# Performance work log

Measured on AMD Instinct MI355X. Metric: run time of the kernel, lower is better.

## Reference

```python
import jax, jax.numpy as jnp
import numpy as np

B, S, F, L = 128, 512, 128, 1024  # batch, seq_len, n_features, latent_dim


def _gru_step(h, x, W_ih, W_hh, b_ih, b_hh):
    # PyTorch GRUCell math, gate order (r, z, n)
    gi = x @ W_ih.T + b_ih            # [B, 3L]
    gh = h @ W_hh.T + b_hh            # [B, 3L]
    ir, iz, inn = jnp.split(gi, 3, axis=-1)
    hr, hz, hn = jnp.split(gh, 3, axis=-1)
    r = jax.nn.sigmoid(ir + hr)
    z = jax.nn.sigmoid(iz + hz)
    n = jnp.tanh(inn + r * hn)
    return (1.0 - z) * n + z * h


def setup_inputs() -> dict:
    key = jax.random.key(0)
    ks = jax.random.split(key, 12)
    s_e = 1.0 / np.sqrt(L)
    u = lambda k, shape: jax.random.uniform(k, shape, jnp.float32, -s_e, s_e)
    return {
        "x": jax.random.normal(ks[0], (B, S, F), jnp.float32),
        # encoder GRU (single layer)
        "W_ih_e": u(ks[1], (3 * L, F)),
        "W_hh_e": u(ks[2], (3 * L, L)),
        "b_ih_e": u(ks[3], (3 * L,)),
        "b_hh_e": u(ks[4], (3 * L,)),
        # decoder GRUCell
        "W_ih_d": u(ks[5], (3 * L, F)),
        "W_hh_d": u(ks[6], (3 * L, L)),
        "b_ih_d": u(ks[7], (3 * L,)),
        "b_hh_d": u(ks[8], (3 * L,)),
        # decoder Linear(latent_dim -> n_features)
        "W_out": u(ks[9], (F, L)),
        "b_out": u(ks[10], (F,)),
    }


def reference(x, W_ih_e, W_hh_e, b_ih_e, b_hh_e,
              W_ih_d, W_hh_d, b_ih_d, b_hh_d, W_out, b_out):
    seq_len = x.shape[1]

    # ---- encoder: GRU over time, return final hidden state h_n [B, L] ----
    def enc_step(h, x_t):
        h = _gru_step(h, x_t, W_ih_e, W_hh_e, b_ih_e, b_hh_e)
        return h, None

    h0 = jnp.zeros((x.shape[0], W_hh_e.shape[1]), x.dtype)
    h_n, _ = jax.lax.scan(enc_step, h0, jnp.swapaxes(x, 0, 1))  # scan over [S,B,F]

    # ---- decoder: GRUCell + Linear unrolled seq_len steps ----
    x_init = h_n @ W_out.T + b_out  # [B, F]

    def dec_step(carry, _):
        h, x_i = carry
        h = _gru_step(h, x_i, W_ih_d, W_hh_d, b_ih_d, b_hh_d)
        x_i = h @ W_out.T + b_out
        return (h, x_i), x_i

    _, xs = jax.lax.scan(dec_step, (h_n, x_init), None, length=seq_len)  # [S,B,F]
    out = jnp.swapaxes(xs, 0, 1)  # [B,S,F]
    return jnp.flip(out, axis=1)
```

## Files before the change

kernel.cpp:

```cpp
#include <hip/hip_runtime.h>
#include <hip/hip_bf16.h>


#define B_ 128
#define S_ 512
#define F_ 128
#define L_ 1024
#define U_ 8
#define NWG_E 128
#define NWG_D 144

typedef __bf16 bf16x8 __attribute__((ext_vector_type(8)));
typedef float  f32x4  __attribute__((ext_vector_type(4)));
typedef float  f32x16 __attribute__((ext_vector_type(16)));
typedef int    i32x4  __attribute__((ext_vector_type(4)));
typedef unsigned long long u64;

union pk2 { unsigned u; __bf16 h[2]; };
union fu  { float f; unsigned u; };

#define MFMA32(a, b, c) __builtin_amdgcn_mfma_f32_32x32x16_bf16(a, b, c, 0, 0, 0)
#define Z16 f32x16{0.f,0.f,0.f,0.f,0.f,0.f,0.f,0.f,0.f,0.f,0.f,0.f,0.f,0.f,0.f,0.f}

#define LDG16(dst, p) asm volatile("global_load_dwordx4 %0, %1, off sc0 sc1" : "=v"(dst) : "v"(p))
#define VMWAIT16(a) asm volatile("s_waitcnt vmcnt(0)" \
    : "+v"(a[0]),"+v"(a[1]),"+v"(a[2]),"+v"(a[3]),"+v"(a[4]),"+v"(a[5]),"+v"(a[6]),"+v"(a[7]), \
      "+v"(a[8]),"+v"(a[9]),"+v"(a[10]),"+v"(a[11]),"+v"(a[12]),"+v"(a[13]),"+v"(a[14]),"+v"(a[15]) \
    :: "memory")
#define SB0() __builtin_amdgcn_sched_barrier(0)

#define O_H0   0
#define O_H1   (256*1024)
#define O_H32  (512*1024)
#define O_CTR  (1024*1024)
#define O_ZERO_END (1024*1024 + 8192)
#define O_XB   O_ZERO_END
#define O_WEH  (O_XB  + 16777216)
#define O_WEX  (O_WEH + 8388608)
#define O_BE   (O_WEX + 1048576)
#define O_WD   (O_BE  + 16384)
#define O_BD   (O_WD  + 8388608)
#define O_WC   (O_BD  + 16384)
#define O_WOB  (O_WC  + 6291456)


__global__ void k_xcvt(const float* __restrict__ x, __bf16* __restrict__ xb, int n) {
    int i = blockIdx.x * 256 + threadIdx.x;
    int stride = gridDim.x * 256;
    for (; i < n; i += stride) xb[i] = (__bf16)x[i];
}

__global__ void k_woutb(const float* __restrict__ Wout, __bf16* __restrict__ Wob, int n) {
    int i = blockIdx.x * 256 + threadIdx.x;
    if (i < n) Wob[i] = (__bf16)Wout[i];
}

__global__ void k_pack_enc(const float* __restrict__ Wih, const float* __restrict__ Whh,
                           const float* __restrict__ bih, const float* __restrict__ bhh,
                           __bf16* __restrict__ Weh, __bf16* __restrict__ Wex,
                           float* __restrict__ be) {
    int g = blockIdx.x, tid = threadIdx.x;
    for (int i = tid; i < 32 * 1024; i += 256) {
        int c = i >> 10, k = i & 1023;
        int u = g * U_ + (c >> 2), gate = c & 3;
        float v = 0.f;
        if (gate == 0)      v = Whh[(size_t)u * 1024 + k];
        else if (gate == 1) v = Whh[(size_t)(1024 + u) * 1024 + k];
        else if (gate == 3) v = Whh[(size_t)(2048 + u) * 1024 + k];
        Weh[((size_t)g * 32 + c) * 1024 + k] = (__bf16)v;
    }
    for (int i = tid; i < 32 * 128; i += 256) {
        int c = i >> 7, k = i & 127;
        int u = g * U_ + (c >> 2), gate = c & 3;
        float v = 0.f;
        if (gate == 0)      v = Wih[(size_t)u * 128 + k];
        else if (gate == 1) v = Wih[(size_t)(1024 + u) * 128 + k];
        else if (gate == 2) v = Wih[(size_t)(2048 + u) * 128 + k];
        Wex[((size_t)g * 32 + c) * 128 + k] = (__bf16)v;
    }
    if (tid < 32) {
        int c = tid, u = g * U_ + (c >> 2), gate = c & 3;
        float v;
        if (gate == 0)      v = bih[u] + bhh[u];
        else if (gate == 1) v = bih[1024 + u] + bhh[1024 + u];
        else if (gate == 2) v = bih[2048 + u];
        else                v = bhh[2048 + u];
        be[g * 32 + c] = v;
    }
}

__global__ void k_wcomb(const float* __restrict__ Wihd, const float* __restrict__ Wout,
                        __bf16* __restrict__ Wc) {
    __shared__ float a[8][128];
    int r0 = blockIdx.x * 8, tid = threadIdx.x;
    for (int i = tid; i < 8 * 128; i += 256)
        a[i >> 7][i & 127] = Wihd[(size_t)(r0 + (i >> 7)) * 128 + (i & 127)];
    __syncthreads();
    for (int j = tid; j < 1024; j += 256) {
        float acc[8] = {0, 0, 0, 0, 0, 0, 0, 0};
        for (int f = 0; f < 128; ++f) {
            float w = Wout[(size_t)f * 1024 + j];
#pragma unroll
            for (int r = 0; r < 8; ++r) acc[r] += a[r][f] * w;
        }
        for (int r = 0; r < 8; ++r) Wc[(size_t)(r0 + r) * 1024 + j] = (__bf16)acc[r];
    }
}

__global__ void k_pack_dec(const float* __restrict__ Whhd, const __bf16* __restrict__ Wc,
                           const float* __restrict__ Wihd,
                           const float* __restrict__ bihd, const float* __restrict__ bhhd,
                           const float* __restrict__ bout,
                           __bf16* __restrict__ Wd, float* __restrict__ bd) {
    int g = blockIdx.x, tid = threadIdx.x;
    for (int i = tid; i < 32 * 1024; i += 256) {
        int c = i >> 10, k = i & 1023;
        int u = g * U_ + (c >> 2), gate = c & 3;
        float v;
        if (gate == 0)      v = Whhd[(size_t)u * 1024 + k] + (float)Wc[(size_t)u * 1024 + k];
        else if (gate == 1) v = Whhd[(size_t)(1024 + u) * 1024 + k] + (float)Wc[(size_t)(1024 + u) * 1024 + k];
        else if (gate == 2) v = (float)Wc[(size_t)(2048 + u) * 1024 + k];
        else                v = Whhd[(size_t)(2048 + u) * 1024 + k];
        Wd[((size_t)g * 32 + c) * 1024 + k] = (__bf16)v;
    }
    if (tid < 32) {
        int c = tid;
        int u = g * U_ + (c >> 2), gate = c & 3;
        int row = (gate == 0) ? u : (gate == 1) ? (1024 + u) : (2048 + u);
        float v;
        if (gate <= 1) {
            float d = 0.f;
            for (int f = 0; f < 128; ++f) d += Wihd[(size_t)row * 128 + f] * bout[f];
            v = d + bihd[row] + bhhd[row];
        } else if (gate == 2) {
            float d = 0.f;
            for (int f = 0; f < 128; ++f) d += Wihd[(size_t)row * 128 + f] * bout[f];
            v = d + bihd[row];
        } else {
            v = bhhd[row];
        }
        bd[g * 32 + c] = v;
    }
}


__device__ __forceinline__ void bar_arrive(unsigned* base, int g) {
    if (threadIdx.x == 0)
        __hip_atomic_fetch_add(base + (g & 15) * 32, 1u,
                               __ATOMIC_RELAXED, __HIP_MEMORY_SCOPE_AGENT);
}

__device__ __forceinline__ void bar_wait(unsigned* base, unsigned tgt) {
    if (threadIdx.x == 0) {
        for (;;) {
            unsigned sum = 0;
#pragma unroll
            for (int j = 0; j < 16; ++j)
                sum += __hip_atomic_load(base + j * 32, __ATOMIC_RELAXED, __HIP_MEMORY_SCOPE_AGENT);
            if (sum >= tgt) break;
            __builtin_amdgcn_s_sleep(1);
        }
    }
    __syncthreads();
}

__global__ __launch_bounds__(512, 2) void k_enc(
    const __bf16* __restrict__ xb, const __bf16* __restrict__ Weh,
    const __bf16* __restrict__ Wex, const float* __restrict__ be,
    __bf16* __restrict__ h0, __bf16* __restrict__ h1,
    float* __restrict__ h32, unsigned* __restrict__ ctr) {
    __shared__ __align__(16) __bf16 sWh[32][1032];
    __shared__ __align__(16) __bf16 sWx[32][136];
    __shared__ float sB[32];
    __shared__ __align__(16) float sGa[128][36];
    __shared__ __align__(16) float sGb[128][36];
    const int g = blockIdx.x, tid = threadIdx.x;
    const int lane = tid & 63, wave = tid >> 6;

    for (int i = tid; i < 32 * 128; i += 512) {
        int c = i >> 7, k8 = i & 127;
        *(i32x4*)&sWh[c][k8 * 8] = *(const i32x4*)(Weh + ((size_t)g * 32 + c) * 1024 + k8 * 8);
    }
    for (int i = tid; i < 32 * 16; i += 512) {
        int c = i >> 4, k8 = i & 15;
        *(i32x4*)&sWx[c][k8 * 8] = *(const i32x4*)(Wex + ((size_t)g * 32 + c) * 128 + k8 * 8);
    }
    if (tid < 32) sB[tid] = be[g * 32 + tid];
    __syncthreads();

    const int bcol = lane & 31;
    const int koff = (lane >> 5) * 8;
    const int mrow = (wave & 3) * 32 + bcol;
    const int kb = (wave >> 2) * 32;
    const bool up = (wave >= 4);

    bf16x8 xrg[8];
    if (up) {
#pragma unroll
        for (int kt = 0; kt < 8; ++kt) xrg[kt] = *(const bf16x8*)(&sWx[bcol][kt * 16 + koff]);
    }

    const int erow = tid >> 2, pair = tid & 3;
    const int hidx2 = g * 512 + erow * 4 + pair;
    float ha = 0.f, hb = 0.f;

    f32x16 accx = Z16;
    if (up) {
        const __bf16* xr = xb + (size_t)mrow * 65536;
#pragma unroll
        for (int kt = 0; kt < 8; ++kt)
            accx = MFMA32(*(const bf16x8*)(xr + kt * 16 + koff), xrg[kt], accx);
    }

    for (int s = 0; s < 512; ++s) {
        const __bf16* hcur = (s & 1) ? h1 : h0;
        __bf16* hnxt = (s & 1) ? h0 : h1;
        {
            f32x16 aA = up ? accx : Z16;
            f32x16 aB = Z16;
            const __bf16* hr = hcur + ((size_t)(kb * 2 + (koff >> 3)) << 10) + mrow * 8;
            bf16x8 af[16];
#pragma unroll
            for (int i = 0; i < 16; ++i) LDG16(af[i], hr + i * 2048);
            VMWAIT16(af); SB0();
#pragma unroll
            for (int i = 0; i < 16; ++i) {
                const bf16x8 b = *(const bf16x8*)(&sWh[bcol][(kb + i) * 16 + koff]);
                if (i & 1) aB = MFMA32(af[i], b, aB); else aA = MFMA32(af[i], b, aA);
                LDG16(af[i], hr + (16 + i) * 2048);
            }
            VMWAIT16(af); SB0();
#pragma unroll
            for (int i = 0; i < 16; ++i) {
                const bf16x8 b = *(const bf16x8*)(&sWh[bcol][(kb + 16 + i) * 16 + koff]);
                if (i & 1) aB = MFMA32(af[i], b, aB); else aA = MFMA32(af[i], b, aA);
            }
            f32x16 acc = aA + aB;
            int rb = (wave & 3) * 32 + 4 * (lane >> 5);
            float (*sg)[36] = up ? sGb : sGa;
#pragma unroll
            for (int r = 0; r < 16; ++r)
                sg[rb + (r & 3) + 8 * (r >> 2)][bcol] = acc[r];
        }
        __syncthreads();
        {
            f32x4 g0 = *(const f32x4*)&sGa[erow][pair * 8] + *(const f32x4*)&sGb[erow][pair * 8];
            f32x4 g1 = *(const f32x4*)&sGa[erow][pair * 8 + 4] + *(const f32x4*)&sGb[erow][pair * 8 + 4];
            int c0 = pair * 8;
            float r = 1.f / (1.f + __expf(-(g0[0] + sB[c0 + 0])));
            float z = 1.f / (1.f + __expf(-(g0[1] + sB[c0 + 1])));
            float n = tanhf(g0[2] + sB[c0 + 2] + r * (g0[3] + sB[c0 + 3]));
            ha = (1.f - z) * n + z * ha;
            r = 1.f / (1.f + __expf(-(g1[0] + sB[c0 + 4])));
            z = 1.f / (1.f + __expf(-(g1[1] + sB[c0 + 5])));
            n = tanhf(g1[2] + sB[c0 + 6] + r * (g1[3] + sB[c0 + 7]));
            hb = (1.f - z) * n + z * hb;
            pk2 p; p.h[0] = (__bf16)ha; p.h[1] = (__bf16)hb;
            __hip_atomic_store((unsigned*)hnxt + hidx2, p.u, __ATOMIC_RELAXED, __HIP_MEMORY_SCOPE_AGENT);
            if (s == 511) {
                h32[erow * 1024 + g * 8 + pair * 2]     = ha;
                h32[erow * 1024 + g * 8 + pair * 2 + 1] = hb;
            }
        }
        if (s < 511) {
            __syncthreads();
            bar_arrive(ctr, g);
            if (up) {
                f32x16 ax = Z16;
                const __bf16* xr = xb + (size_t)mrow * 65536 + (size_t)(s + 1) * 128;
#pragma unroll
                for (int kt = 0; kt < 8; ++kt)
                    ax = MFMA32(*(const bf16x8*)(xr + kt * 16 + koff), xrg[kt], ax);
                accx = ax;
            }
            bar_wait(ctr, (unsigned)(s + 1) * NWG_E);
        }
    }
}

__global__ __launch_bounds__(512, 2) void k_dec(
    const __bf16* __restrict__ Wd, const float* __restrict__ bd,
    const __bf16* __restrict__ Wob, const float* __restrict__ bout,
    __bf16* __restrict__ h0, __bf16* __restrict__ h1,
    const float* __restrict__ h32, float* __restrict__ out,
    unsigned* __restrict__ ctr) {
    __shared__ __align__(16) __bf16 sW[32][1032];
    __shared__ float sB[32];
    __shared__ __align__(16) float sGa[128][36];
    __shared__ __align__(16) float sGb[128][36];
    const int g = blockIdx.x, tid = threadIdx.x;
    const int lane = tid & 63, wave = tid >> 6;
    const bool gwg = (g < 128);
    const int go = g - 128;

    if (gwg) {
        for (int i = tid; i < 32 * 128; i += 512) {
            int c = i >> 7, k8 = i & 127;
            *(i32x4*)&sW[c][k8 * 8] = *(const i32x4*)(Wd + ((size_t)g * 32 + c) * 1024 + k8 * 8);
        }
        if (tid < 32) sB[tid] = bd[g * 32 + tid];
    } else {
        for (int i = tid; i < 32 * 128; i += 512) {
            int c = i >> 7, k8 = i & 127;
            *(i32x4*)&sW[c][k8 * 8] =
                *(const i32x4*)(Wob + ((size_t)((go >> 2) * 32 + c)) * 1024 + k8 * 8);
        }
        if (tid < 32) sB[tid] = bout[(go >> 2) * 32 + tid];
    }
    __syncthreads();

    const int bcol = lane & 31;
    const int koff = (lane >> 5) * 8;
    const int kb = (wave >> 2) * 32;
    const bool up = (wave >= 4);
    const int arow = gwg ? ((wave & 3) * 32 + bcol)
                         : ((go & 3) * 32 + bcol);

    const int erow = tid >> 2, pair = tid & 3;
    const int hidx2 = g * 512 + erow * 4 + pair;
    float ha = 0.f, hb = 0.f;
    if (gwg) {
        ha = h32[erow * 1024 + g * 8 + pair * 2];
        hb = h32[erow * 1024 + g * 8 + pair * 2 + 1];
    }

    if (gwg) {
        for (int s = 0; s < 512; ++s) {
            const __bf16* hcur = (s & 1) ? h1 : h0;
            __bf16* hnxt = (s & 1) ? h0 : h1;
            {
                f32x16 aA = Z16, aB = Z16;
                const __bf16* hr = hcur + ((size_t)(kb * 2 + (koff >> 3)) << 10) + arow * 8;
                bf16x8 af[16];
#pragma unroll
                for (int i = 0; i < 16; ++i) LDG16(af[i], hr + i * 2048);
                VMWAIT16(af); SB0();
#pragma unroll
                for (int i = 0; i < 16; ++i) {
                    const bf16x8 b = *(const bf16x8*)(&sW[bcol][(kb + i) * 16 + koff]);
                    if (i & 1) aB = MFMA32(af[i], b, aB); else aA = MFMA32(af[i], b, aA);
                    LDG16(af[i], hr + (16 + i) * 2048);
                }
                VMWAIT16(af); SB0();
#pragma unroll
                for (int i = 0; i < 16; ++i) {
                    const bf16x8 b = *(const bf16x8*)(&sW[bcol][(kb + 16 + i) * 16 + koff]);
                    if (i & 1) aB = MFMA32(af[i], b, aB); else aA = MFMA32(af[i], b, aA);
                }
                f32x16 acc = aA + aB;
                int rb = (wave & 3) * 32 + 4 * (lane >> 5);
                float (*sg)[36] = up ? sGb : sGa;
#pragma unroll
                for (int r = 0; r < 16; ++r)
                    sg[rb + (r & 3) + 8 * (r >> 2)][bcol] = acc[r];
            }
            __syncthreads();
            {
                f32x4 g0 = *(const f32x4*)&sGa[erow][pair * 8] + *(const f32x4*)&sGb[erow][pair * 8];
                f32x4 g1 = *(const f32x4*)&sGa[erow][pair * 8 + 4] + *(const f32x4*)&sGb[erow][pair * 8 + 4];
                int c0 = pair * 8;
                float r = 1.f / (1.f + __expf(-(g0[0] + sB[c0 + 0])));
                float z = 1.f / (1.f + __expf(-(g0[1] + sB[c0 + 1])));
                float n = tanhf(g0[2] + sB[c0 + 2] + r * (g0[3] + sB[c0 + 3]));
                ha = (1.f - z) * n + z * ha;
                r = 1.f / (1.f + __expf(-(g1[0] + sB[c0 + 4])));
                z = 1.f / (1.f + __expf(-(g1[1] + sB[c0 + 5])));
                n = tanhf(g1[2] + sB[c0 + 6] + r * (g1[3] + sB[c0 + 7]));
                hb = (1.f - z) * n + z * hb;
                pk2 p; p.h[0] = (__bf16)ha; p.h[1] = (__bf16)hb;
                __hip_atomic_store((unsigned*)hnxt + hidx2, p.u, __ATOMIC_RELAXED, __HIP_MEMORY_SCOPE_AGENT);
            }
            __syncthreads();
            bar_arrive(ctr, g);
            if (s < 511) bar_wait(ctr, (unsigned)(s + 1) * NWG_D);
        }
    } else {
        __shared__ __align__(16) float sGo[4][32][32];
        for (int s = 0; s <= 512; ++s) {
            const __bf16* hcur = (s & 1) ? h1 : h0;
            const bool cmp = (wave < 4) && (s >= 1);
            if (cmp) {
                f32x16 aA = Z16, aB = Z16;
                const __bf16* hr = hcur + ((size_t)(wave * 32 + (koff >> 3)) << 10) + arow * 8;
                bf16x8 af[16];
#pragma unroll
                for (int i = 0; i < 16; ++i) LDG16(af[i], hr + i * 2048);
                VMWAIT16(af); SB0();
#pragma unroll
                for (int i = 0; i < 16; ++i) {
                    const bf16x8 b = *(const bf16x8*)(&sW[bcol][(wave * 16 + i) * 16 + koff]);
                    if (i & 1) aB = MFMA32(af[i], b, aB); else aA = MFMA32(af[i], b, aA);
                }
                f32x16 acc = aA + aB;
                int rb = 4 * (lane >> 5);
#pragma unroll
                for (int r = 0; r < 16; ++r)
                    sGo[wave][rb + (r & 3) + 8 * (r >> 2)][bcol] = acc[r];
            }
            __syncthreads();
            if (s < 512) bar_arrive(ctr, g);
            if (s >= 1) {
                int c = tid & 31, r0 = (tid >> 5) & 15;
#pragma unroll
                for (int hh = 0; hh < 2; ++hh) {
                    int r = r0 + hh * 16;
                    fu cv;
                    cv.f = sGo[0][r][c] + sGo[1][r][c] + sGo[2][r][c] + sGo[3][r][c] + sB[c];
                    size_t off = ((size_t)((go & 3) * 32 + r) * 512 + (size_t)(512 - s)) * 128
                               + (go >> 2) * 32 + c;
                    __hip_atomic_store((unsigned*)(out + off), cv.u,
                                       __ATOMIC_RELAXED, __HIP_MEMORY_SCOPE_AGENT);
                }
            }
            if (s < 512) bar_wait(ctr, (unsigned)(s + 1) * NWG_D);
        }
    }
}

extern "C" void kernel_launch(void* const* d_in, const int* in_sizes, int n_in,
                              void* d_out, int out_size, void* d_ws, size_t ws_size,
                              hipStream_t stream) {
    (void)in_sizes; (void)n_in; (void)out_size; (void)ws_size;
    const float* x    = (const float*)d_in[0];
    const float* Wihe = (const float*)d_in[1];
    const float* Whhe = (const float*)d_in[2];
    const float* bihe = (const float*)d_in[3];
    const float* bhhe = (const float*)d_in[4];
    const float* Wihd = (const float*)d_in[5];
    const float* Whhd = (const float*)d_in[6];
    const float* bihd = (const float*)d_in[7];
    const float* bhhd = (const float*)d_in[8];
    const float* Wout = (const float*)d_in[9];
    const float* bout = (const float*)d_in[10];

    char* ws = (char*)d_ws;
    __bf16*   h0  = (__bf16*)(ws + O_H0);
    __bf16*   h1  = (__bf16*)(ws + O_H1);
    float*    h32 = (float*)(ws + O_H32);
    unsigned* ctr = (unsigned*)(ws + O_CTR);
    __bf16*   xbf = (__bf16*)(ws + O_XB);
    __bf16*   Weh = (__bf16*)(ws + O_WEH);
    __bf16*   Wex = (__bf16*)(ws + O_WEX);
    float*    be  = (float*)(ws + O_BE);
    __bf16*   Wd  = (__bf16*)(ws + O_WD);
    float*    bd  = (float*)(ws + O_BD);
    __bf16*   Wc  = (__bf16*)(ws + O_WC);
    __bf16*   Wob = (__bf16*)(ws + O_WOB);

    hipMemsetAsync(ws, 0, O_ZERO_END, stream);

    k_xcvt<<<4096, 256, 0, stream>>>(x, xbf, B_ * S_ * F_);
    k_pack_enc<<<NWG_E, 256, 0, stream>>>(Wihe, Whhe, bihe, bhhe, Weh, Wex, be);
    k_wcomb<<<384, 256, 0, stream>>>(Wihd, Wout, Wc);
    k_pack_dec<<<NWG_E, 256, 0, stream>>>(Whhd, Wc, Wihd, bihd, bhhd, bout, Wd, bd);
    k_woutb<<<512, 256, 0, stream>>>(Wout, Wob, F_ * L_);

    k_enc<<<NWG_E, 512, 0, stream>>>(xbf, Weh, Wex, be, h0, h1, h32, ctr);
    k_dec<<<NWG_D, 512, 0, stream>>>(Wd, bd, Wob, bout, h0, h1, h32, (float*)d_out,
                                     ctr + 1024);
}
```

Before: 6.005 ms.

## Split batch across two workgroups per column group and fuse output projection into decoder

Encoder and decoder kernels now launch 256 workgroups, each handling half the batch (64 rows) for one 32-column gate group, so every wave does one 16-step K slice instead of 32. The decoder drops its dedicated output-projection workgroups: each workgroup computes one output feature with a dot product on the h fragments it already loaded, using per-wave Wout registers and a small shared reduction. This halves per-step MFMA and load work per workgroup, at the cost of twice as many participants in the grid barrier and duplicated weight staging.

```diff
diff --git a/kernel.cpp b/kernel.cpp
--- a/kernel.cpp
+++ b/kernel.cpp
@@ -6,15 +6,12 @@
 #define S_ 512
 #define F_ 128
 #define L_ 1024
-#define U_ 8
-#define NWG_E 128
-#define NWG_D 144
+#define NWG 256
 
 typedef __bf16 bf16x8 __attribute__((ext_vector_type(8)));
 typedef float  f32x4  __attribute__((ext_vector_type(4)));
 typedef float  f32x16 __attribute__((ext_vector_type(16)));
 typedef int    i32x4  __attribute__((ext_vector_type(4)));
-typedef unsigned long long u64;
 
 union pk2 { unsigned u; __bf16 h[2]; };
 union fu  { float f; unsigned u; };
@@ -62,7 +59,7 @@
     int g = blockIdx.x, tid = threadIdx.x;
     for (int i = tid; i < 32 * 1024; i += 256) {
         int c = i >> 10, k = i & 1023;
-        int u = g * U_ + (c >> 2), gate = c & 3;
+        int u = g * 8 + (c >> 2), gate = c & 3;
         float v = 0.f;
         if (gate == 0)      v = Whh[(size_t)u * 1024 + k];
         else if (gate == 1) v = Whh[(size_t)(1024 + u) * 1024 + k];
@@ -71,7 +68,7 @@
     }
     for (int i = tid; i < 32 * 128; i += 256) {
         int c = i >> 7, k = i & 127;
-        int u = g * U_ + (c >> 2), gate = c & 3;
+        int u = g * 8 + (c >> 2), gate = c & 3;
         float v = 0.f;
         if (gate == 0)      v = Wih[(size_t)u * 128 + k];
         else if (gate == 1) v = Wih[(size_t)(1024 + u) * 128 + k];
@@ -79,7 +76,7 @@
         Wex[((size_t)g * 32 + c) * 128 + k] = (__bf16)v;
     }
     if (tid < 32) {
-        int c = tid, u = g * U_ + (c >> 2), gate = c & 3;
+        int c = tid, u = g * 8 + (c >> 2), gate = c & 3;
         float v;
         if (gate == 0)      v = bih[u] + bhh[u];
         else if (gate == 1) v = bih[1024 + u] + bhh[1024 + u];
@@ -115,7 +112,7 @@
     int g = blockIdx.x, tid = threadIdx.x;
     for (int i = tid; i < 32 * 1024; i += 256) {
         int c = i >> 10, k = i & 1023;
-        int u = g * U_ + (c >> 2), gate = c & 3;
+        int u = g * 8 + (c >> 2), gate = c & 3;
         float v;
         if (gate == 0)      v = Whhd[(size_t)u * 1024 + k] + (float)Wc[(size_t)u * 1024 + k];
         else if (gate == 1) v = Whhd[(size_t)(1024 + u) * 1024 + k] + (float)Wc[(size_t)(1024 + u) * 1024 + k];
@@ -125,7 +122,7 @@
     }
     if (tid < 32) {
         int c = tid;
-        int u = g * U_ + (c >> 2), gate = c & 3;
+        int u = g * 8 + (c >> 2), gate = c & 3;
         int row = (gate == 0) ? u : (gate == 1) ? (1024 + u) : (2048 + u);
         float v;
         if (gate <= 1) {
@@ -172,108 +169,89 @@
     __shared__ __align__(16) __bf16 sWh[32][1032];
     __shared__ __align__(16) __bf16 sWx[32][136];
     __shared__ float sB[32];
-    __shared__ __align__(16) float sGa[128][36];
-    __shared__ __align__(16) float sGb[128][36];
+    __shared__ __align__(16) float sG[4][64][36];
     const int g = blockIdx.x, tid = threadIdx.x;
     const int lane = tid & 63, wave = tid >> 6;
+    const int cg = g & 127, rg = g >> 7;
 
     for (int i = tid; i < 32 * 128; i += 512) {
         int c = i >> 7, k8 = i & 127;
-        *(i32x4*)&sWh[c][k8 * 8] = *(const i32x4*)(Weh + ((size_t)g * 32 + c) * 1024 + k8 * 8);
+        *(i32x4*)&sWh[c][k8 * 8] = *(const i32x4*)(Weh + ((size_t)cg * 32 + c) * 1024 + k8 * 8);
     }
     for (int i = tid; i < 32 * 16; i += 512) {
         int c = i >> 4, k8 = i & 15;
-        *(i32x4*)&sWx[c][k8 * 8] = *(const i32x4*)(Wex + ((size_t)g * 32 + c) * 128 + k8 * 8);
-    }
-    if (tid < 32) sB[tid] = be[g * 32 + tid];
+        *(i32x4*)&sWx[c][k8 * 8] = *(const i32x4*)(Wex + ((size_t)cg * 32 + c) * 128 + k8 * 8);
+    }
+    if (tid < 32) sB[tid] = be[cg * 32 + tid];
     __syncthreads();
 
     const int bcol = lane & 31;
     const int koff = (lane >> 5) * 8;
-    const int mrow = (wave & 3) * 32 + bcol;
-    const int kb = (wave >> 2) * 32;
-    const bool up = (wave >= 4);
-
-    bf16x8 xrg[8];
-    if (up) {
-#pragma unroll
-        for (int kt = 0; kt < 8; ++kt) xrg[kt] = *(const bf16x8*)(&sWx[bcol][kt * 16 + koff]);
-    }
-
-    const int erow = tid >> 2, pair = tid & 3;
-    const int hidx2 = g * 512 + erow * 4 + pair;
-    float ha = 0.f, hb = 0.f;
+    const int rs = wave & 1, ks = wave >> 1;
+    const int grow = rg * 64 + rs * 32 + bcol;
+
+    const int lrow = tid >> 3, up = tid & 7;
+    const int growg = rg * 64 + lrow;
+    float hst = 0.f;
 
     f32x16 accx = Z16;
-    if (up) {
-        const __bf16* xr = xb + (size_t)mrow * 65536;
-#pragma unroll
-        for (int kt = 0; kt < 8; ++kt)
-            accx = MFMA32(*(const bf16x8*)(xr + kt * 16 + koff), xrg[kt], accx);
+    {
+        const __bf16* xr = xb + (size_t)grow * 65536;
+#pragma unroll
+        for (int i = 0; i < 2; ++i) {
+            int kx = ks * 2 + i;
+            bf16x8 a = *(const bf16x8*)(xr + kx * 16 + koff);
+            accx = MFMA32(a, *(const bf16x8*)(&sWx[bcol][kx * 16 + koff]), accx);
+        }
     }
 
     for (int s = 0; s < 512; ++s) {
         const __bf16* hcur = (s & 1) ? h1 : h0;
         __bf16* hnxt = (s & 1) ? h0 : h1;
         {
-            f32x16 aA = up ? accx : Z16;
-            f32x16 aB = Z16;
-            const __bf16* hr = hcur + ((size_t)(kb * 2 + (koff >> 3)) << 10) + mrow * 8;
+            f32x16 acc = accx;
+            const __bf16* hr = hcur + ((size_t)(ks * 32 + (koff >> 3)) << 10) + grow * 8;
             bf16x8 af[16];
 #pragma unroll
             for (int i = 0; i < 16; ++i) LDG16(af[i], hr + i * 2048);
             VMWAIT16(af); SB0();
 #pragma unroll
-            for (int i = 0; i < 16; ++i) {
-                const bf16x8 b = *(const bf16x8*)(&sWh[bcol][(kb + i) * 16 + koff]);
-                if (i & 1) aB = MFMA32(af[i], b, aB); else aA = MFMA32(af[i], b, aA);
-                LDG16(af[i], hr + (16 + i) * 2048);
-            }
-            VMWAIT16(af); SB0();
-#pragma unroll
-            for (int i = 0; i < 16; ++i) {
-                const bf16x8 b = *(const bf16x8*)(&sWh[bcol][(kb + 16 + i) * 16 + koff]);
-                if (i & 1) aB = MFMA32(af[i], b, aB); else aA = MFMA32(af[i], b, aA);
-            }
-            f32x16 acc = aA + aB;
-            int rb = (wave & 3) * 32 + 4 * (lane >> 5);
-            float (*sg)[36] = up ? sGb : sGa;
+            for (int i = 0; i < 16; ++i)
+                acc = MFMA32(af[i], *(const bf16x8*)(&sWh[bcol][(ks * 16 + i) * 16 + koff]), acc);
+            int rb = rs * 32 + 4 * (lane >> 5);
 #pragma unroll
             for (int r = 0; r < 16; ++r)
-                sg[rb + (r & 3) + 8 * (r >> 2)][bcol] = acc[r];
+                sG[ks][rb + (r & 3) + 8 * (r >> 2)][bcol] = acc[r];
         }
         __syncthreads();
         {
-            f32x4 g0 = *(const f32x4*)&sGa[erow][pair * 8] + *(const f32x4*)&sGb[erow][pair * 8];
-            f32x4 g1 = *(const f32x4*)&sGa[erow][pair * 8 + 4] + *(const f32x4*)&sGb[erow][pair * 8 + 4];
-            int c0 = pair * 8;
-            float r = 1.f / (1.f + __expf(-(g0[0] + sB[c0 + 0])));
-            float z = 1.f / (1.f + __expf(-(g0[1] + sB[c0 + 1])));
-            float n = tanhf(g0[2] + sB[c0 + 2] + r * (g0[3] + sB[c0 + 3]));
-            ha = (1.f - z) * n + z * ha;
-            r = 1.f / (1.f + __expf(-(g1[0] + sB[c0 + 4])));
-            z = 1.f / (1.f + __expf(-(g1[1] + sB[c0 + 5])));
-            n = tanhf(g1[2] + sB[c0 + 6] + r * (g1[3] + sB[c0 + 7]));
-            hb = (1.f - z) * n + z * hb;
-            pk2 p; p.h[0] = (__bf16)ha; p.h[1] = (__bf16)hb;
-            __hip_atomic_store((unsigned*)hnxt + hidx2, p.u, __ATOMIC_RELAXED, __HIP_MEMORY_SCOPE_AGENT);
-            if (s == 511) {
-                h32[erow * 1024 + g * 8 + pair * 2]     = ha;
-                h32[erow * 1024 + g * 8 + pair * 2 + 1] = hb;
+            int c0 = up * 4;
+            f32x4 v = *(const f32x4*)&sG[0][lrow][c0] + *(const f32x4*)&sG[1][lrow][c0]
+                    + *(const f32x4*)&sG[2][lrow][c0] + *(const f32x4*)&sG[3][lrow][c0];
+            float r = 1.f / (1.f + __expf(-(v[0] + sB[c0 + 0])));
+            float z = 1.f / (1.f + __expf(-(v[1] + sB[c0 + 1])));
+            float n = tanhf(v[2] + sB[c0 + 2] + r * (v[3] + sB[c0 + 3]));
+            hst = (1.f - z) * n + z * hst;
+            float hnb = __shfl_down(hst, 1);
+            if ((up & 1) == 0) {
+                pk2 p; p.h[0] = (__bf16)hst; p.h[1] = (__bf16)hnb;
+                __hip_atomic_store((unsigned*)hnxt + cg * 512 + growg * 4 + (up >> 1), p.u,
+                                   __ATOMIC_RELAXED, __HIP_MEMORY_SCOPE_AGENT);
             }
+            if (s == 511) h32[growg * 1024 + cg * 8 + up] = hst;
         }
         if (s < 511) {
             __syncthreads();
             bar_arrive(ctr, g);
-            if (up) {
-                f32x16 ax = Z16;
-                const __bf16* xr = xb + (size_t)mrow * 65536 + (size_t)(s + 1) * 128;
-#pragma unroll
-                for (int kt = 0; kt < 8; ++kt)
-                    ax = MFMA32(*(const bf16x8*)(xr + kt * 16 + koff), xrg[kt], ax);
-                accx = ax;
+            accx = Z16;
+            const __bf16* xr = xb + (size_t)grow * 65536 + (size_t)(s + 1) * 128;
+#pragma unroll
+            for (int i = 0; i < 2; ++i) {
+                int kx = ks * 2 + i;
+                bf16x8 a = *(const bf16x8*)(xr + kx * 16 + koff);
+                accx = MFMA32(a, *(const bf16x8*)(&sWx[bcol][kx * 16 + koff]), accx);
             }
-            bar_wait(ctr, (unsigned)(s + 1) * NWG_E);
+            bar_wait(ctr, (unsigned)(s + 1) * NWG);
         }
     }
 }
@@ -286,133 +264,92 @@
     unsigned* __restrict__ ctr) {
     __shared__ __align__(16) __bf16 sW[32][1032];
     __shared__ float sB[32];
-    __shared__ __align__(16) float sGa[128][36];
-    __shared__ __align__(16) float sGb[128][36];
+    __shared__ __align__(16) float sG[4][64][36];
+    __shared__ float sOd[2][32][4];
     const int g = blockIdx.x, tid = threadIdx.x;
     const int lane = tid & 63, wave = tid >> 6;
-    const bool gwg = (g < 128);
-    const int go = g - 128;
-
-    if (gwg) {
-        for (int i = tid; i < 32 * 128; i += 512) {
-            int c = i >> 7, k8 = i & 127;
-            *(i32x4*)&sW[c][k8 * 8] = *(const i32x4*)(Wd + ((size_t)g * 32 + c) * 1024 + k8 * 8);
-        }
-        if (tid < 32) sB[tid] = bd[g * 32 + tid];
-    } else {
-        for (int i = tid; i < 32 * 128; i += 512) {
-            int c = i >> 7, k8 = i & 127;
-            *(i32x4*)&sW[c][k8 * 8] =
-                *(const i32x4*)(Wob + ((size_t)((go >> 2) * 32 + c)) * 1024 + k8 * 8);
-        }
-        if (tid < 32) sB[tid] = bout[(go >> 2) * 32 + tid];
-    }
+    const int cg = g & 127, rg = g >> 7;
+
+    for (int i = tid; i < 32 * 128; i += 512) {
+        int c = i >> 7, k8 = i & 127;
+        *(i32x4*)&sW[c][k8 * 8] = *(const i32x4*)(Wd + ((size_t)cg * 32 + c) * 1024 + k8 * 8);
+    }
+    if (tid < 32) sB[tid] = bd[cg * 32 + tid];
     __syncthreads();
 
     const int bcol = lane & 31;
     const int koff = (lane >> 5) * 8;
-    const int kb = (wave >> 2) * 32;
-    const bool up = (wave >= 4);
-    const int arow = gwg ? ((wave & 3) * 32 + bcol)
-                         : ((go & 3) * 32 + bcol);
-
-    const int erow = tid >> 2, pair = tid & 3;
-    const int hidx2 = g * 512 + erow * 4 + pair;
-    float ha = 0.f, hb = 0.f;
-    if (gwg) {
-        ha = h32[erow * 1024 + g * 8 + pair * 2];
-        hb = h32[erow * 1024 + g * 8 + pair * 2 + 1];
-    }
-
-    if (gwg) {
-        for (int s = 0; s < 512; ++s) {
-            const __bf16* hcur = (s & 1) ? h1 : h0;
-            __bf16* hnxt = (s & 1) ? h0 : h1;
-            {
-                f32x16 aA = Z16, aB = Z16;
-                const __bf16* hr = hcur + ((size_t)(kb * 2 + (koff >> 3)) << 10) + arow * 8;
-                bf16x8 af[16];
-#pragma unroll
-                for (int i = 0; i < 16; ++i) LDG16(af[i], hr + i * 2048);
-                VMWAIT16(af); SB0();
-#pragma unroll
-                for (int i = 0; i < 16; ++i) {
-                    const bf16x8 b = *(const bf16x8*)(&sW[bcol][(kb + i) * 16 + koff]);
-                    if (i & 1) aB = MFMA32(af[i], b, aB); else aA = MFMA32(af[i], b, aA);
-                    LDG16(af[i], hr + (16 + i) * 2048);
-                }
-                VMWAIT16(af); SB0();
-#pragma unroll
-                for (int i = 0; i < 16; ++i) {
-                    const bf16x8 b = *(const bf16x8*)(&sW[bcol][(kb + 16 + i) * 16 + koff]);
-                    if (i & 1) aB = MFMA32(af[i], b, aB); else aA = MFMA32(af[i], b, aA);
-                }
-                f32x16 acc = aA + aB;
-                int rb = (wave & 3) * 32 + 4 * (lane >> 5);
-                float (*sg)[36] = up ? sGb : sGa;
-#pragma unroll
-                for (int r = 0; r < 16; ++r)
-                    sg[rb + (r & 3) + 8 * (r >> 2)][bcol] = acc[r];
+    const int rs = wave & 1, ks = wave >> 1;
+    const int grow = rg * 64 + rs * 32 + bcol;
+
+    const int lrow = tid >> 3, up = tid & 7;
+    const int growg = rg * 64 + lrow;
+    float hst = h32[growg * 1024 + cg * 8 + up];
+    const float ob = bout[cg];
+
+    bf16x8 wf[16];
+#pragma unroll
+    for (int i = 0; i < 16; ++i)
+        wf[i] = *(const bf16x8*)(Wob + (size_t)cg * 1024 + (ks * 16 + i) * 16 + koff);
+
+    for (int s = 0; s <= 512; ++s) {
+        const __bf16* hcur = (s & 1) ? h1 : h0;
+        __bf16* hnxt = (s & 1) ? h0 : h1;
+        bf16x8 af[16];
+        {
+            const __bf16* hr = hcur + ((size_t)(ks * 32 + (koff >> 3)) << 10) + grow * 8;
+#pragma unroll
+            for (int i = 0; i < 16; ++i) LDG16(af[i], hr + i * 2048);
+            VMWAIT16(af); SB0();
+        }
+        if (s < 512) {
+            f32x16 acc = Z16;
+#pragma unroll
+            for (int i = 0; i < 16; ++i)
+                acc = MFMA32(af[i], *(const bf16x8*)(&sW[bcol][(ks * 16 + i) * 16 + koff]), acc);
+            int rb = rs * 32 + 4 * (lane >> 5);
+#pragma unroll
+            for (int r = 0; r < 16; ++r)
+                sG[ks][rb + (r & 3) + 8 * (r >> 2)][bcol] = acc[r];
+        }
+        if (s >= 1) {
+            float pd = 0.f;
+#pragma unroll
+            for (int i = 0; i < 16; ++i)
+#pragma unroll
+                for (int j = 0; j < 8; ++j)
+                    pd += (float)af[i][j] * (float)wf[i][j];
+            pd += __shfl_xor(pd, 32);
+            if (lane < 32) sOd[rs][bcol][ks] = pd;
+        }
+        __syncthreads();
+        if (s < 512) {
+            int c0 = up * 4;
+            f32x4 v = *(const f32x4*)&sG[0][lrow][c0] + *(const f32x4*)&sG[1][lrow][c0]
+                    + *(const f32x4*)&sG[2][lrow][c0] + *(const f32x4*)&sG[3][lrow][c0];
+            float r = 1.f / (1.f + __expf(-(v[0] + sB[c0 + 0])));
+            float z = 1.f / (1.f + __expf(-(v[1] + sB[c0 + 1])));
+            float n = tanhf(v[2] + sB[c0 + 2] + r * (v[3] + sB[c0 + 3]));
+            hst = (1.f - z) * n + z * hst;
+            float hnb = __shfl_down(hst, 1);
+            if ((up & 1) == 0) {
+                pk2 p; p.h[0] = (__bf16)hst; p.h[1] = (__bf16)hnb;
+                __hip_atomic_store((unsigned*)hnxt + cg * 512 + growg * 4 + (up >> 1), p.u,
+                                   __ATOMIC_RELAXED, __HIP_MEMORY_SCOPE_AGENT);
             }
-            __syncthreads();
-            {
-                f32x4 g0 = *(const f32x4*)&sGa[erow][pair * 8] + *(const f32x4*)&sGb[erow][pair * 8];
-                f32x4 g1 = *(const f32x4*)&sGa[erow][pair * 8 + 4] + *(const f32x4*)&sGb[erow][pair * 8 + 4];
-                int c0 = pair * 8;
-                float r = 1.f / (1.f + __expf(-(g0[0] + sB[c0 + 0])));
-                float z = 1.f / (1.f + __expf(-(g0[1] + sB[c0 + 1])));
-                float n = tanhf(g0[2] + sB[c0 + 2] + r * (g0[3] + sB[c0 + 3]));
-                ha = (1.f - z) * n + z * ha;
-                r = 1.f / (1.f + __expf(-(g1[0] + sB[c0 + 4])));
-                z = 1.f / (1.f + __expf(-(g1[1] + sB[c0 + 5])));
-                n = tanhf(g1[2] + sB[c0 + 6] + r * (g1[3] + sB[c0 + 7]));
-                hb = (1.f - z) * n + z * hb;
-                pk2 p; p.h[0] = (__bf16)ha; p.h[1] = (__bf16)hb;
-                __hip_atomic_store((unsigned*)hnxt + hidx2, p.u, __ATOMIC_RELAXED, __HIP_MEMORY_SCOPE_AGENT);
-            }
+        }
+        if (s >= 1 && tid < 64) {
+            int rr = tid & 31, rss = tid >> 5;
+            float val = sOd[rss][rr][0] + sOd[rss][rr][1] + sOd[rss][rr][2] + sOd[rss][rr][3] + ob;
+            fu cv; cv.f = val;
+            int growo = rg * 64 + rss * 32 + rr;
+            __hip_atomic_store((unsigned*)(out + (size_t)growo * 65536 + (size_t)(512 - s) * 128 + cg),
+                               cv.u, __ATOMIC_RELAXED, __HIP_MEMORY_SCOPE_AGENT);
+        }
+        if (s < 512) {
             __syncthreads();
             bar_arrive(ctr, g);
-            if (s < 511) bar_wait(ctr, (unsigned)(s + 1) * NWG_D);
-        }
-    } else {
-        __shared__ __align__(16) float sGo[4][32][32];
-        for (int s = 0; s <= 512; ++s) {
-            const __bf16* hcur = (s & 1) ? h1 : h0;
-            const bool cmp = (wave < 4) && (s >= 1);
-            if (cmp) {
-                f32x16 aA = Z16, aB = Z16;
-                const __bf16* hr = hcur + ((size_t)(wave * 32 + (koff >> 3)) << 10) + arow * 8;
-                bf16x8 af[16];
-#pragma unroll
-                for (int i = 0; i < 16; ++i) LDG16(af[i], hr + i * 2048);
-                VMWAIT16(af); SB0();
-#pragma unroll
-                for (int i = 0; i < 16; ++i) {
-                    const bf16x8 b = *(const bf16x8*)(&sW[bcol][(wave * 16 + i) * 16 + koff]);
-                    if (i & 1) aB = MFMA32(af[i], b, aB); else aA = MFMA32(af[i], b, aA);
-                }
-                f32x16 acc = aA + aB;
-                int rb = 4 * (lane >> 5);
-#pragma unroll
-                for (int r = 0; r < 16; ++r)
-                    sGo[wave][rb + (r & 3) + 8 * (r >> 2)][bcol] = acc[r];
-            }
-            __syncthreads();
-            if (s < 512) bar_arrive(ctr, g);
-            if (s >= 1) {
-                int c = tid & 31, r0 = (tid >> 5) & 15;
-#pragma unroll
-                for (int hh = 0; hh < 2; ++hh) {
-                    int r = r0 + hh * 16;
-                    fu cv;
-                    cv.f = sGo[0][r][c] + sGo[1][r][c] + sGo[2][r][c] + sGo[3][r][c] + sB[c];
-                    size_t off = ((size_t)((go & 3) * 32 + r) * 512 + (size_t)(512 - s)) * 128
-                               + (go >> 2) * 32 + c;
-                    __hip_atomic_store((unsigned*)(out + off), cv.u,
-                                       __ATOMIC_RELAXED, __HIP_MEMORY_SCOPE_AGENT);
-                }
-            }
-            if (s < 512) bar_wait(ctr, (unsigned)(s + 1) * NWG_D);
+            bar_wait(ctr, (unsigned)(s + 1) * NWG);
         }
     }
 }
@@ -450,12 +387,12 @@
     hipMemsetAsync(ws, 0, O_ZERO_END, stream);
 
     k_xcvt<<<4096, 256, 0, stream>>>(x, xbf, B_ * S_ * F_);
-    k_pack_enc<<<NWG_E, 256, 0, stream>>>(Wihe, Whhe, bihe, bhhe, Weh, Wex, be);
+    k_pack_enc<<<128, 256, 0, stream>>>(Wihe, Whhe, bihe, bhhe, Weh, Wex, be);
     k_wcomb<<<384, 256, 0, stream>>>(Wihd, Wout, Wc);
-    k_pack_dec<<<NWG_E, 256, 0, stream>>>(Whhd, Wc, Wihd, bihd, bhhd, bout, Wd, bd);
+    k_pack_dec<<<128, 256, 0, stream>>>(Whhd, Wc, Wihd, bihd, bhhd, bout, Wd, bd);
     k_woutb<<<512, 256, 0, stream>>>(Wout, Wob, F_ * L_);
 
-    k_enc<<<NWG_E, 512, 0, stream>>>(xbf, Weh, Wex, be, h0, h1, h32, ctr);
-    k_dec<<<NWG_D, 512, 0, stream>>>(Wd, bd, Wob, bout, h0, h1, h32, (float*)d_out,
-                                     ctr + 1024);
-}
+    k_enc<<<NWG, 512, 0, stream>>>(xbf, Weh, Wex, be, h0, h1, h32, ctr);
+    k_dec<<<NWG, 512, 0, stream>>>(Wd, bd, Wob, bout, h0, h1, h32, (float*)d_out,
+                                   ctr + 1024);
+}
```

Result: faster. 5.144 ms (-14.3%).
